# Optimization experiments

Hardware: AMD Instinct MI355X
Metric: run time of the kernel (lower is better)

The kernel has to match this reference:

```python
import jax, jax.numpy as jnp
import numpy as np
import math

B, T, D, N = 4, 1024, 768, 7  # batch, seq, d_model, n_chambers
STEP, WARMUP = 4000, 2000      # curriculum: step past warmup -> all masks ~1
INIT_SCALE = 0.01


def _curriculum_masks():
    # NautilusScheduler.get_masks: smooth sigmoid activation per chamber (static floats)
    slope = 8.0 * N / WARMUP
    return [1.0 / (1.0 + math.exp(-slope * (STEP - WARMUP * (i + 0.5) / N))) for i in range(N)]


def _layernorm(x, g, b, eps=1e-5):
    m = jnp.mean(x, axis=-1, keepdims=True)
    v = jnp.mean((x - m) ** 2, axis=-1, keepdims=True)
    return (x - m) * jax.lax.rsqrt(v + eps) * g + b


def _chamber(h, Wq, Wk, gw, gb, sp, mask_val, causal):
    # get_bias stand-in: bilinear content bias (B,T,T)
    q = h @ Wq                                   # (B,T,D)
    k = h @ Wk                                   # (B,T,D)
    bias = jnp.einsum('btd,bsd->bts', q, k) / jnp.sqrt(jnp.asarray(D, h.dtype))
    bias = jnp.where(causal[None], bias, -jnp.inf)   # causal masked_fill
    w = jnp.nan_to_num(jax.nn.softmax(bias, axis=-1))
    enrichment = jnp.einsum('bts,bsd->btd', w, h) - h
    gate = jax.nn.sigmoid(h @ gw[:, None] + gb)      # (B,T,1)
    scale = jax.nn.softplus(sp)                      # learnable positive scale
    return scale * gate * mask_val * enrichment


def setup_inputs() -> dict:
    key = jax.random.key(0)
    ks = jax.random.split(key, 8)
    x = jax.random.normal(ks[0], (B, T, D), jnp.float32)
    s = 1.0 / np.sqrt(D)
    Wq = jax.random.normal(ks[1], (N, D, D), jnp.float32) * s
    Wk = jax.random.normal(ks[2], (N, D, D), jnp.float32) * s
    gate_w = jax.random.normal(ks[3], (N, D), jnp.float32) * 0.02
    gate_b = jnp.zeros((N,), jnp.float32)
    # per-chamber softplus-inverse init: log(exp(init*(1+3*prog))-1+1e-6)
    sp = np.array([math.log(math.exp(INIT_SCALE * (1.0 + 3.0 * i / (N - 1))) - 1.0 + 1e-6)
                   for i in range(N)], dtype=np.float32)
    scale_p = jnp.asarray(sp)
    merge_W = jax.random.normal(ks[4], (D, N * D), jnp.float32) * (1.0 / np.sqrt(N * D))
    return {
        'x': x, 'Wq': Wq, 'Wk': Wk, 'gate_w': gate_w, 'gate_b': gate_b,
        'scale_p': scale_p, 'merge_W': merge_W,
        'mode_logit': jnp.float32(0.0), 'residual_gate': jnp.float32(0.1),
        'ln_pre_g': jnp.ones((D,), jnp.float32), 'ln_pre_b': jnp.zeros((D,), jnp.float32),
        'ln_post_g': jnp.ones((D,), jnp.float32), 'ln_post_b': jnp.zeros((D,), jnp.float32),
    }


def reference(x, Wq, Wk, gate_w, gate_b, scale_p, merge_W, mode_logit,
              residual_gate, ln_pre_g, ln_pre_b, ln_post_g, ln_post_b):
    masks = _curriculum_masks()
    causal = jnp.tril(jnp.ones((T, T), bool))
    h = _layernorm(x, ln_pre_g, ln_pre_b)
    mode_gate = jax.nn.sigmoid(mode_logit)
    seq = jnp.zeros_like(h)
    deltas = []
    for i in range(N):  # fixed small structural loop over chambers
        seq = seq + _chamber(h + seq, Wq[i], Wk[i], gate_w[i], gate_b[i],
                             scale_p[i], masks[i], causal)
        deltas.append(_chamber(h, Wq[i], Wk[i], gate_w[i], gate_b[i],
                               scale_p[i], masks[i], causal))
    par = jnp.concatenate(deltas, axis=-1) @ merge_W.T  # (B,T,D)
    enrichment = (1.0 - mode_gate) * seq + mode_gate * par
    enrichment = _layernorm(enrichment, ln_post_g, ln_post_b)
    return x + residual_gate * enrichment
```

## Files before the change

kernel.cpp:

```cpp
#include <hip/hip_runtime.h>
#include <hip/hip_bf16.h>
#include <math.h>

#define D_MODEL 768
#define T_SEQ   1024
#define BATCH   4
#define NCH     7
#define ROWS    4096
#define KM      (NCH * D_MODEL)

typedef unsigned short u16;
typedef __attribute__((ext_vector_type(8))) short bh8;
typedef __attribute__((ext_vector_type(4))) float f32x4;

__device__ __forceinline__ u16 f2bf(float f) {
    union { float f; unsigned u; } v; v.f = f;
    return (u16)((v.u + 0x7fffu + ((v.u >> 16) & 1u)) >> 16);
}
__device__ __forceinline__ float bf2f(u16 b) {
    union { unsigned u; float f; } v; v.u = ((unsigned)b) << 16;
    return v.f;
}
__device__ __forceinline__ float wred_sum(float v) {
    #pragma unroll
    for (int o = 32; o; o >>= 1) v += __shfl_down(v, o, 64);
    return v;
}
__device__ __forceinline__ float wred_max(float v) {
    #pragma unroll
    for (int o = 32; o; o >>= 1) v = fmaxf(v, __shfl_down(v, o, 64));
    return v;
}
__device__ __forceinline__ float chamber_mask(int i) {
    float slope = 8.0f * 7.0f / 2000.0f;
    return 1.0f / (1.0f + __expf(-slope * (4000.0f - 2000.0f * (i + 0.5f) / 7.0f)));
}

#define GLD16(g, l) __builtin_amdgcn_global_load_lds( \
    (const __attribute__((address_space(1))) void*)(g), \
    (__attribute__((address_space(3))) void*)(l), 16, 0, 0)

__device__ __forceinline__ int xcd_swizzle(int gflat, int Ntot) {
    if ((Ntot & 7) == 0) {
        int chunk = Ntot >> 3;
        gflat = (gflat & 7) * chunk + (gflat >> 3);
    }
    return gflat;
}

__global__ __launch_bounds__(256)
void gemm_nt_kernel(const u16* __restrict__ A, const u16* __restrict__ B,
                    void* __restrict__ Cv,
                    int K, int lda, int ldb, int ldc,
                    long long sA1, long long sA2, long long sB1, long long sB2,
                    long long sC1, long long sC2, int zm,
                    float alpha, int mode, int causal_skip, int causal_k,
                    int kss, int klen)
{
    int gx = gridDim.x, gy = gridDim.y;
    int Ntot = gx * gy * gridDim.z;
    int gflat = xcd_swizzle(blockIdx.x + gx * (blockIdx.y + gy * blockIdx.z), Ntot);
    int bn = gflat % gx;
    int rest = gflat / gx;
    int bm = rest % gy;
    int bz = rest / gy;
    if (causal_skip && bn > bm) return;
    int bz1 = bz % zm, bz2 = bz / zm;

    const u16* Ab = A + bz1 * sA1 + bz2 * sA2 + (long long)(bm * 128) * lda;
    const u16* Bb = B + bz1 * sB1 + bz2 * sB2 + (long long)(bn * 128) * ldb;

    __shared__ u16 sm[4 * 128 * 32];
    u16* Al0 = sm;
    u16* Bl0 = sm + 128 * 32;
    u16* Al1 = sm + 2 * 128 * 32;
    u16* Bl1 = sm + 3 * 128 * 32;

    int tid  = threadIdx.x;
    int lane = tid & 63;
    int wave = tid >> 6;
    int wm = wave >> 1, wn = wave & 1;

    int k_begin = kss ? bz1 * kss : 0;
    int k_end   = klen ? (k_begin + klen) : K;
    if (causal_k) k_end = min(k_end, (bm + 1) * 128);

    f32x4 acc[4][4];
    #pragma unroll
    for (int i = 0; i < 4; i++)
        #pragma unroll
        for (int j = 0; j < 4; j++)
            acc[i][j] = (f32x4){0.f, 0.f, 0.f, 0.f};

    int srow = lane >> 2;
    int skq  = (lane & 3) * 8;
    int fm   = lane & 15;
    int fk   = (lane >> 4) * 8;

    for (int k0 = k_begin; k0 < k_end; k0 += 64) {
        __syncthreads();
        #pragma unroll
        for (int r = 0; r < 2; r++) {
            int row = r * 64 + wave * 16 + srow;
            long long ra = (long long)row * lda + k0 + skq;
            long long rb2 = (long long)row * ldb + k0 + skq;
            GLD16(Ab + ra,       Al0 + row * 32 + skq);
            GLD16(Bb + rb2,      Bl0 + row * 32 + skq);
            GLD16(Ab + ra + 32,  Al1 + row * 32 + skq);
            GLD16(Bb + rb2 + 32, Bl1 + row * 32 + skq);
        }
        __syncthreads();

        #pragma unroll
        for (int p = 0; p < 2; p++) {
            const u16* Al = p ? Al1 : Al0;
            const u16* Bl = p ? Bl1 : Bl0;
            bh8 af[4], bf[4];
            #pragma unroll
            for (int i = 0; i < 4; i++)
                af[i] = *(const bh8*)(Al + (wm * 64 + i * 16 + fm) * 32 + fk);
            #pragma unroll
            for (int j = 0; j < 4; j++)
                bf[j] = *(const bh8*)(Bl + (wn * 64 + j * 16 + fm) * 32 + fk);
            #pragma unroll
            for (int i = 0; i < 4; i++)
                #pragma unroll
                for (int j = 0; j < 4; j++)
                    acc[i][j] = __builtin_amdgcn_mfma_f32_16x16x32_bf16(af[i], bf[j], acc[i][j], 0, 0, 0);
        }
    }

    int rbase = bm * 128 + wm * 64 + (lane >> 4) * 4;
    int cbase = bn * 128 + wn * 64 + (lane & 15);
    long long zoff = bz1 * sC1 + bz2 * sC2;
    if (mode == 1) {
        u16* C = (u16*)Cv + zoff;
        #pragma unroll
        for (int i = 0; i < 4; i++)
            #pragma unroll
            for (int j = 0; j < 4; j++)
                #pragma unroll
                for (int r = 0; r < 4; r++)
                    C[(long long)(rbase + i * 16 + r) * ldc + cbase + j * 16] = f2bf(acc[i][j][r] * alpha);
    } else if (mode == 3) {
        u16* C = (u16*)Cv + zoff;
        #pragma unroll
        for (int i = 0; i < 4; i++)
            #pragma unroll
            for (int j = 0; j < 4; j++)
                #pragma unroll
                for (int r = 0; r < 4; r++) {
                    union { _Float16 h; u16 u; } cv;
                    cv.h = (_Float16)(acc[i][j][r] * alpha);
                    C[(long long)(rbase + i * 16 + r) * ldc + cbase + j * 16] = cv.u;
                }
    } else {
        float* C = (float*)Cv + zoff;
        #pragma unroll
        for (int i = 0; i < 4; i++)
            #pragma unroll
            for (int j = 0; j < 4; j++)
                #pragma unroll
                for (int r = 0; r < 4; r++)
                    C[(long long)(rbase + i * 16 + r) * ldc + cbase + j * 16] = acc[i][j][r] * alpha;
    }
}

__global__ __launch_bounds__(256)
void gemm64_nt_kernel(const u16* __restrict__ A, const u16* __restrict__ B,
                      void* __restrict__ Cv,
                      int K, int lda, int ldb, int ldc,
                      long long sA1, long long sA2, long long sB1, long long sB2,
                      long long sC1, long long sC2, int zm,
                      float alpha, int mode, int causal_skip, int causal_k,
                      float* __restrict__ hhfp, const float* __restrict__ coefp,
                      u16* __restrict__ hbsp, u16* __restrict__ htsp,
                      const float* __restrict__ hp, u16* __restrict__ dbp)
{
    int gx = gridDim.x, gy = gridDim.y;
    int Ntot = gx * gy * gridDim.z;
    int gflat = xcd_swizzle(blockIdx.x + gx * (blockIdx.y + gy * blockIdx.z), Ntot);
    int bn = gflat % gx;
    int rest = gflat / gx;
    int bm = rest % gy;
    int bz = rest / gy;
    if (causal_skip && bn > bm) return;
    int bz1 = bz % zm, bz2 = bz / zm;

    const u16* Ab = A + bz1 * sA1 + bz2 * sA2 + (long long)(bm * 64) * lda;
    const u16* Bb = B + bz1 * sB1 + bz2 * sB2 + (long long)(bn * 64) * ldb;

    __shared__ u16 sm[8 * 64 * 32];
    const int PS = 64 * 32;

    int tid  = threadIdx.x;
    int lane = tid & 63;
    int wave = tid >> 6;

    int k_end = causal_k ? min(K, (bm + 1) * 64) : K;

    f32x4 acc[4];
    #pragma unroll
    for (int j = 0; j < 4; j++) acc[j] = (f32x4){0.f, 0.f, 0.f, 0.f};

    int srow   = tid >> 2;
    int schunk = (tid & 3) * 8;
    int fm     = lane & 15;
    int fk     = (lane >> 4) * 8;

    int k0 = 0;
    while (k0 < k_end) {
        __syncthreads();
        if (k_end - k0 >= 128) {
            #pragma unroll
            for (int p = 0; p < 4; p++) {
                long long ra  = (long long)srow * lda + k0 + p * 32 + schunk;
                long long rb2 = (long long)srow * ldb + k0 + p * 32 + schunk;
                GLD16(Ab + ra,  sm + (2 * p) * PS + srow * 32 + schunk);
                GLD16(Bb + rb2, sm + (2 * p + 1) * PS + srow * 32 + schunk);
            }
            __syncthreads();
            #pragma unroll
            for (int p = 0; p < 4; p++) {
                const u16* Al = sm + (2 * p) * PS;
                const u16* Bl = sm + (2 * p + 1) * PS;
                bh8 af = *(const bh8*)(Al + (wave * 16 + fm) * 32 + fk);
                bh8 bf[4];
                #pragma unroll
                for (int j = 0; j < 4; j++)
                    bf[j] = *(const bh8*)(Bl + (j * 16 + fm) * 32 + fk);
                #pragma unroll
                for (int j = 0; j < 4; j++)
                    acc[j] = __builtin_amdgcn_mfma_f32_16x16x32_bf16(af, bf[j], acc[j], 0, 0, 0);
            }
            k0 += 128;
        } else {
            #pragma unroll
            for (int p = 0; p < 2; p++) {
                long long ra  = (long long)srow * lda + k0 + p * 32 + schunk;
                long long rb2 = (long long)srow * ldb + k0 + p * 32 + schunk;
                GLD16(Ab + ra,  sm + (2 * p) * PS + srow * 32 + schunk);
                GLD16(Bb + rb2, sm + (2 * p + 1) * PS + srow * 32 + schunk);
            }
            __syncthreads();
            #pragma unroll
            for (int p = 0; p < 2; p++) {
                const u16* Al = sm + (2 * p) * PS;
                const u16* Bl = sm + (2 * p + 1) * PS;
                bh8 af = *(const bh8*)(Al + (wave * 16 + fm) * 32 + fk);
                bh8 bf[4];
                #pragma unroll
                for (int j = 0; j < 4; j++)
                    bf[j] = *(const bh8*)(Bl + (j * 16 + fm) * 32 + fk);
                #pragma unroll
                for (int j = 0; j < 4; j++)
                    acc[j] = __builtin_amdgcn_mfma_f32_16x16x32_bf16(af, bf[j], acc[j], 0, 0, 0);
            }
            k0 += 64;
        }
    }

    int rbase = bm * 64 + wave * 16 + (lane >> 4) * 4;
    int cbase = bn * 64 + (lane & 15);
    long long zoff = bz1 * sC1 + bz2 * sC2;
    if (mode == 1) {
        u16* C = (u16*)Cv + zoff;
        #pragma unroll
        for (int j = 0; j < 4; j++)
            #pragma unroll
            for (int r = 0; r < 4; r++)
                C[(long long)(rbase + r) * ldc + cbase + j * 16] = f2bf(acc[j][r] * alpha);
    } else if (mode == 3) {
        u16* C = (u16*)Cv + zoff;
        #pragma unroll
        for (int j = 0; j < 4; j++)
            #pragma unroll
            for (int r = 0; r < 4; r++) {
                union { _Float16 h; u16 u; } cv;
                cv.h = (_Float16)(acc[j][r] * alpha);
                C[(long long)(rbase + r) * ldc + cbase + j * 16] = cv.u;
            }
    } else if (mode == 5) {
        int b = bz1, ch = bz2;
        #pragma unroll
        for (int r = 0; r < 4; r++) {
            int t = rbase + r;
            long long rowg = (long long)b * T_SEQ + t;
            float cf = coefp[(long long)ch * ROWS + rowg];
            #pragma unroll
            for (int j = 0; j < 4; j++) {
                int d = cbase + j * 16;
                float hv = hp[rowg * D_MODEL + d];
                dbp[rowg * KM + ch * D_MODEL + d] = f2bf(cf * (acc[j][r] - hv));
            }
        }
    } else if (mode == 6) {
        __syncthreads();
        u16* tile = sm;
        #pragma unroll
        for (int r = 0; r < 4; r++) {
            int t = rbase + r;
            long long rowg = (long long)bz1 * T_SEQ + t;
            float cf = coefp[rowg];
            int tl = t - bm * 64;
            #pragma unroll
            for (int j = 0; j < 4; j++) {
                int d = cbase + j * 16;
                long long idx = rowg * D_MODEL + d;
                float v = hhfp[idx];
                float nh = v + cf * (acc[j][r] - v);
                hhfp[idx] = nh;
                u16 w = f2bf(nh);
                hbsp[idx] = w;
                tile[((lane & 15) + j * 16) * 66 + tl] = w;
            }
        }
        __syncthreads();
        int dl = tid >> 2, tch = (tid & 3) * 16;
        long long ob = (long long)bz1 * T_SEQ * D_MODEL +
                       (long long)(bn * 64 + dl) * T_SEQ + bm * 64 + tch;
        #pragma unroll
        for (int kk = 0; kk < 16; kk++)
            htsp[ob + kk] = tile[dl * 66 + tch + kk];
    } else {
        float* C = (float*)Cv + zoff;
        #pragma unroll
        for (int j = 0; j < 4; j++)
            #pragma unroll
            for (int r = 0; r < 4; r++)
                C[(long long)(rbase + r) * ldc + cbase + j * 16] = acc[j][r] * alpha;
    }
}

__global__ __launch_bounds__(256)
void ln_pre_kernel(const float* __restrict__ x, const float* __restrict__ g,
                   const float* __restrict__ b, float* __restrict__ h,
                   float* __restrict__ hhf, u16* __restrict__ hbp,
                   u16* __restrict__ hbs)
{
    int row = blockIdx.x;
    long long base = (long long)row * D_MODEL;
    int tid = threadIdx.x, lane = tid & 63, wave = tid >> 6;
    __shared__ float red[4];
    float v[3]; float s = 0.f;
    #pragma unroll
    for (int k = 0; k < 3; k++) { v[k] = x[base + tid + k * 256]; s += v[k]; }
    s = wred_sum(s);
    if (lane == 0) red[wave] = s;
    __syncthreads();
    float mean = (red[0] + red[1] + red[2] + red[3]) * (1.f / D_MODEL);
    __syncthreads();
    float sq = 0.f;
    #pragma unroll
    for (int k = 0; k < 3; k++) { float dd = v[k] - mean; sq += dd * dd; }
    sq = wred_sum(sq);
    if (lane == 0) red[wave] = sq;
    __syncthreads();
    float var = (red[0] + red[1] + red[2] + red[3]) * (1.f / D_MODEL);
    float rstd = rsqrtf(var + 1e-5f);
    #pragma unroll
    for (int k = 0; k < 3; k++) {
        int c = tid + k * 256;
        float o = (v[k] - mean) * rstd * g[c] + b[c];
        h[base + c] = o; hhf[base + c] = o;
        u16 w = f2bf(o);
        hbp[base + c] = w; hbs[base + c] = w;
    }
}

__global__ __launch_bounds__(256)
void transpose2_kernel(const u16* __restrict__ hb, u16* __restrict__ htp,
                       u16* __restrict__ hts)
{
    __shared__ u16 tile[32][33];
    int b = blockIdx.z;
    int d0 = blockIdx.x * 32, t0 = blockIdx.y * 32;
    int tx = threadIdx.x & 31, ty = threadIdx.x >> 5;
    long long bb = (long long)b * T_SEQ * D_MODEL;
    #pragma unroll
    for (int i = 0; i < 32; i += 8)
        tile[ty + i][tx] = hb[bb + (long long)(t0 + ty + i) * D_MODEL + d0 + tx];
    __syncthreads();
    #pragma unroll
    for (int i = 0; i < 32; i += 8) {
        long long o = bb + (long long)(d0 + ty + i) * T_SEQ + t0 + tx;
        u16 w = tile[tx][ty + i];
        htp[o] = w; hts[o] = w;
    }
}

__device__ __forceinline__ void softmax_row(u16* row, int len, int tid, int lane, int wave,
                                            float* red)
{
    float ev[4];
    float m = -3.0e38f;
    #pragma unroll
    for (int k = 0; k < 4; k++) {
        int s = tid + k * 256;
        if (s < len) {
            union { u16 u; _Float16 h; } cv; cv.u = row[s];
            ev[k] = (float)cv.h;
        } else ev[k] = -3.0e38f;
        m = fmaxf(m, ev[k]);
    }
    m = wred_max(m);
    if (lane == 0) red[wave] = m;
    __syncthreads();
    m = fmaxf(fmaxf(red[0], red[1]), fmaxf(red[2], red[3]));
    __syncthreads();
    float sum = 0.f;
    #pragma unroll
    for (int k = 0; k < 4; k++) {
        int s = tid + k * 256;
        float e = (s < len) ? __expf(ev[k] - m) : 0.f;
        ev[k] = e; sum += e;
    }
    sum = wred_sum(sum);
    if (lane == 0) red[wave] = sum;
    __syncthreads();
    sum = red[0] + red[1] + red[2] + red[3];
    float inv = 1.f / sum;
    #pragma unroll
    for (int k = 0; k < 4; k++)
        row[tid + k * 256] = f2bf(ev[k] * inv);
}

__global__ __launch_bounds__(256)
void softmax_kernel(u16* __restrict__ SP)
{
    int t = blockIdx.x, z = blockIdx.y;
    __shared__ float red[4];
    int tid = threadIdx.x, lane = tid & 63, wave = tid >> 6;
    softmax_row(SP + (long long)z * T_SEQ * T_SEQ + (long long)t * T_SEQ,
                t + 1, tid, lane, wave, red);
}

__global__ __launch_bounds__(256)
void softmax_coef_kernel(u16* __restrict__ SP, const float* __restrict__ hhf,
                         const float* __restrict__ gw, const float* __restrict__ gb,
                         const float* __restrict__ sp, int ci,
                         float* __restrict__ coefS)
{
    int t = blockIdx.x, z = blockIdx.y;
    int tid = threadIdx.x, lane = tid & 63, wave = tid >> 6;
    if (z == BATCH) {
        int row = t * 4 + wave;
        long long base = (long long)row * D_MODEL;
        const float* g = gw + ci * D_MODEL;
        float dot = 0.f;
        #pragma unroll
        for (int k = 0; k < 12; k++) dot += hhf[base + lane + 64 * k] * g[lane + 64 * k];
        dot = wred_sum(dot);
        if (lane == 0) {
            float gate = 1.f / (1.f + __expf(-(dot + gb[ci])));
            coefS[row] = log1pf(expf(sp[ci])) * chamber_mask(ci) * gate;
        }
        return;
    }
    __shared__ float red[4];
    softmax_row(SP + (long long)z * T_SEQ * T_SEQ + (long long)t * T_SEQ,
                t + 1, tid, lane, wave, red);
}

__global__ __launch_bounds__(256)
void coef_par_kernel(const float* __restrict__ h, const float* __restrict__ gw,
                     const float* __restrict__ gb, const float* __restrict__ sp,
                     float* __restrict__ coefP)
{
    int row = blockIdx.x * 4 + (threadIdx.x >> 6);
    int lane = threadIdx.x & 63;
    long long base = (long long)row * D_MODEL;
    float hv[12];
    #pragma unroll
    for (int k = 0; k < 12; k++) hv[k] = h[base + lane + 64 * k];
    for (int ci = 0; ci < NCH; ci++) {
        const float* g = gw + ci * D_MODEL;
        float dot = 0.f;
        #pragma unroll
        for (int k = 0; k < 12; k++) dot += hv[k] * g[lane + 64 * k];
        dot = wred_sum(dot);
        if (lane == 0) {
            float gate = 1.f / (1.f + __expf(-(dot + gb[ci])));
            coefP[ci * ROWS + row] = log1pf(expf(sp[ci])) * chamber_mask(ci) * gate;
        }
    }
}

__global__ __launch_bounds__(256)
void cast4_kernel(const float4* __restrict__ in, ushort4* __restrict__ outp, int n4)
{
    int i = blockIdx.x * 256 + threadIdx.x;
    if (i < n4) {
        float4 v = in[i];
        ushort4 o;
        o.x = f2bf(v.x); o.y = f2bf(v.y); o.z = f2bf(v.z); o.w = f2bf(v.w);
        outp[i] = o;
    }
}

__global__ __launch_bounds__(256)
void final_kernel(const float* __restrict__ x, const float* __restrict__ h,
                  const float* __restrict__ hhf, const u16* __restrict__ Pp,
                  const float* __restrict__ mode_logit, const float* __restrict__ residual_gate,
                  const float* __restrict__ g, const float* __restrict__ b,
                  float* __restrict__ out)
{
    const long long RDe = (long long)ROWS * D_MODEL;
    int row = blockIdx.x;
    long long base = (long long)row * D_MODEL;
    int tid = threadIdx.x, lane = tid & 63, wave = tid >> 6;
    __shared__ float red[4];
    float mg = 1.f / (1.f + __expf(-mode_logit[0]));
    float rg = residual_gate[0];
    float e[3]; float s = 0.f;
    #pragma unroll
    for (int k = 0; k < 3; k++) {
        int c = tid + k * 256;
        float p = 0.f;
        #pragma unroll
        for (int z = 0; z < NCH; z++) p += bf2f(Pp[z * RDe + base + c]);
        float v = (1.f - mg) * (hhf[base + c] - h[base + c]) + mg * p;
        e[k] = v; s += v;
    }
    s = wred_sum(s);
    if (lane == 0) red[wave] = s;
    __syncthreads();
    float mean = (red[0] + red[1] + red[2] + red[3]) * (1.f / D_MODEL);
    __syncthreads();
    float sq = 0.f;
    #pragma unroll
    for (int k = 0; k < 3; k++) { float dd = e[k] - mean; sq += dd * dd; }
    sq = wred_sum(sq);
    if (lane == 0) red[wave] = sq;
    __syncthreads();
    float var = (red[0] + red[1] + red[2] + red[3]) * (1.f / D_MODEL);
    float rstd = rsqrtf(var + 1e-5f);
    #pragma unroll
    for (int k = 0; k < 3; k++) {
        int c = tid + k * 256;
        out[base + c] = x[base + c] + rg * ((e[k] - mean) * rstd * g[c] + b[c]);
    }
}

extern "C" void kernel_launch(void* const* d_in, const int* in_sizes, int n_in,
                              void* d_out, int out_size, void* d_ws, size_t ws_size,
                              hipStream_t stream)
{
    (void)in_sizes; (void)n_in; (void)out_size; (void)ws_size;
    const float* x             = (const float*)d_in[0];
    const float* Wq            = (const float*)d_in[1];
    const float* Wk            = (const float*)d_in[2];
    const float* gate_w        = (const float*)d_in[3];
    const float* gate_b        = (const float*)d_in[4];
    const float* scale_p       = (const float*)d_in[5];
    const float* merge_W       = (const float*)d_in[6];
    const float* mode_logit    = (const float*)d_in[7];
    const float* residual_gate = (const float*)d_in[8];
    const float* ln_pre_g      = (const float*)d_in[9];
    const float* ln_pre_b      = (const float*)d_in[10];
    const float* ln_post_g     = (const float*)d_in[11];
    const float* ln_post_b     = (const float*)d_in[12];
    float* out = (float*)d_out;

    const long long DD  = (long long)D_MODEL * D_MODEL;
    const long long TD  = (long long)T_SEQ * D_MODEL;
    const long long TTs = (long long)T_SEQ * T_SEQ;
    const long long RDe = (long long)ROWS * D_MODEL;

    size_t off = 0;
    char* wsb = (char*)d_ws;
    auto alloc = [&](size_t bytes) -> void* {
        void* p = wsb + off; off += (bytes + 255) & ~(size_t)255; return p;
    };
    u16*   Mtb  = (u16*)alloc((size_t)NCH * DD * 2);
    u16*   mgb  = (u16*)alloc((size_t)D_MODEL * KM * 2);
    float* h    = (float*)alloc(RDe * 4);
    float* hhf  = (float*)alloc(RDe * 4);
    u16*   hbp  = (u16*)alloc(RDe * 2);
    u16*   htp  = (u16*)alloc(RDe * 2);
    u16*   hbs  = (u16*)alloc(RDe * 2);
    u16*   hts0 = (u16*)alloc(RDe * 2);
    u16*   hts1 = (u16*)alloc(RDe * 2);
    u16*   Spar = (u16*)alloc((size_t)(NCH * BATCH) * TTs * 2);
    u16*   Sseq = (u16*)alloc((size_t)BATCH * TTs * 2);
    u16*   Upar = (u16*)alloc((size_t)NCH * RDe * 2);
    u16*   Useq = (u16*)alloc(RDe * 2);
    u16*   db   = (u16*)alloc((size_t)ROWS * KM * 2);
    float* coefP= (float*)alloc((size_t)NCH * ROWS * 4);
    float* coefS= (float*)alloc((size_t)ROWS * 4);
    u16*   Wqb  = Spar;
    u16*   Wkb  = Spar + (size_t)NCH * DD;
    u16*   Pp   = Upar;

    const float sc = 1.0f / sqrtf((float)D_MODEL);
    const int N4W = (int)((size_t)NCH * DD) / 4;
    const int N4M = (int)((size_t)D_MODEL * KM) / 4;

    ln_pre_kernel<<<ROWS, 256, 0, stream>>>(x, ln_pre_g, ln_pre_b, h, hhf, hbp, hbs);
    cast4_kernel<<<(N4W + 255) / 256, 256, 0, stream>>>((const float4*)Wq, (ushort4*)Wqb, N4W);
    cast4_kernel<<<(N4W + 255) / 256, 256, 0, stream>>>((const float4*)Wk, (ushort4*)Wkb, N4W);
    cast4_kernel<<<(N4M + 255) / 256, 256, 0, stream>>>((const float4*)merge_W, (ushort4*)mgb, N4M);
    transpose2_kernel<<<dim3(24, 32, BATCH), 256, 0, stream>>>(hbp, htp, hts0);
    coef_par_kernel<<<ROWS / 4, 256, 0, stream>>>(h, gate_w, gate_b, scale_p, coefP);

    gemm_nt_kernel<<<dim3(6, 6, NCH), 256, 0, stream>>>(
        Wkb, Wqb, Mtb, D_MODEL, D_MODEL, D_MODEL, D_MODEL,
        DD, 0, DD, 0, DD, 0, NCH, 1.f, 1, 0, 0, 0, 0);

    gemm_nt_kernel<<<dim3(6, 32, NCH), 256, 0, stream>>>(
        hbp, Mtb, Upar, D_MODEL, D_MODEL, D_MODEL, D_MODEL,
        0, 0, DD, 0, RDe, 0, NCH, 1.f, 1, 0, 0, 0, 0);
    gemm64_nt_kernel<<<dim3(16, 16, BATCH * NCH), 256, 0, stream>>>(
        Upar, hbp, Spar, D_MODEL, D_MODEL, D_MODEL, T_SEQ,
        TD, RDe, TD, 0, TTs, 4 * TTs, BATCH, sc, 3, 1, 0,
        nullptr, nullptr, nullptr, nullptr, nullptr, nullptr);
    softmax_kernel<<<dim3(T_SEQ, BATCH * NCH), 256, 0, stream>>>(Spar);
    gemm64_nt_kernel<<<dim3(12, 16, BATCH * NCH), 256, 0, stream>>>(
        Spar, htp, nullptr, T_SEQ, T_SEQ, T_SEQ, D_MODEL,
        TTs, 4 * TTs, TD, 0, 0, 0, BATCH, 1.f, 5, 0, 1,
        nullptr, coefP, nullptr, nullptr, h, db);
    gemm_nt_kernel<<<dim3(6, 32, NCH), 256, 0, stream>>>(
        db, mgb, Pp, KM, KM, KM, D_MODEL,
        0, 0, 0, 0, RDe, 0, NCH, 1.f, 1, 0, 0, D_MODEL, D_MODEL);

    u16* htsCur = hts0;
    u16* htsNxt = hts1;
    for (int i = 0; i < NCH; i++) {
        gemm64_nt_kernel<<<dim3(12, 64, 1), 256, 0, stream>>>(
            hbs, Mtb + (long long)i * DD, Useq,
            D_MODEL, D_MODEL, D_MODEL, D_MODEL, 0, 0, 0, 0, 0, 0, 1,
            1.f, 1, 0, 0, nullptr, nullptr, nullptr, nullptr, nullptr, nullptr);
        gemm64_nt_kernel<<<dim3(16, 16, BATCH), 256, 0, stream>>>(
            Useq, hbs, Sseq, D_MODEL, D_MODEL, D_MODEL, T_SEQ,
            TD, 0, TD, 0, TTs, 0, BATCH, sc, 3, 1, 0,
            nullptr, nullptr, nullptr, nullptr, nullptr, nullptr);
        softmax_coef_kernel<<<dim3(T_SEQ, BATCH + 1), 256, 0, stream>>>(
            Sseq, hhf, gate_w, gate_b, scale_p, i, coefS);
        gemm64_nt_kernel<<<dim3(12, 16, BATCH), 256, 0, stream>>>(
            Sseq, htsCur, nullptr, T_SEQ, T_SEQ, T_SEQ, D_MODEL,
            TTs, 0, TD, 0, 0, 0, BATCH, 1.f, 6, 0, 1,
            hhf, coefS, hbs, htsNxt, nullptr, nullptr);
        u16* tmp = htsCur; htsCur = htsNxt; htsNxt = tmp;
    }

    final_kernel<<<ROWS, 256, 0, stream>>>(x, h, hhf, Pp, mode_logit, residual_gate,
                                           ln_post_g, ln_post_b, out);
}
```

Measured before the change: 790.7 us.

## Use 32-row GEMM tiles for sequential chamber loop to raise block count

Adds a gemm32_nt_kernel with 32x64 output tiles and a 2x2 wave layout, and uses it for the three GEMMs inside the sequential per-chamber loop, doubling the grid size so these small serial launches fill more compute units. Causal skipping and the causal K bound are adapted to the finer row granularity. The 64-tile kernel's K loop is collapsed into a single runtime-count loop, and its mode 6 path moves to the new kernel. Smaller tiles halve MFMA work per block and lower data reuse, and the non-unrolled p loop may cost some instruction scheduling.

```diff
diff --git a/kernel.cpp b/kernel.cpp
--- a/kernel.cpp
+++ b/kernel.cpp
@@ -173,8 +173,7 @@
                       long long sA1, long long sA2, long long sB1, long long sB2,
                       long long sC1, long long sC2, int zm,
                       float alpha, int mode, int causal_skip, int causal_k,
-                      float* __restrict__ hhfp, const float* __restrict__ coefp,
-                      u16* __restrict__ hbsp, u16* __restrict__ htsp,
+                      const float* __restrict__ coefp,
                       const float* __restrict__ hp, u16* __restrict__ dbp)
 {
     int gx = gridDim.x, gy = gridDim.y;
@@ -211,53 +210,27 @@
     int k0 = 0;
     while (k0 < k_end) {
         __syncthreads();
-        if (k_end - k0 >= 128) {
-            #pragma unroll
-            for (int p = 0; p < 4; p++) {
-                long long ra  = (long long)srow * lda + k0 + p * 32 + schunk;
-                long long rb2 = (long long)srow * ldb + k0 + p * 32 + schunk;
-                GLD16(Ab + ra,  sm + (2 * p) * PS + srow * 32 + schunk);
-                GLD16(Bb + rb2, sm + (2 * p + 1) * PS + srow * 32 + schunk);
-            }
-            __syncthreads();
-            #pragma unroll
-            for (int p = 0; p < 4; p++) {
-                const u16* Al = sm + (2 * p) * PS;
-                const u16* Bl = sm + (2 * p + 1) * PS;
-                bh8 af = *(const bh8*)(Al + (wave * 16 + fm) * 32 + fk);
-                bh8 bf[4];
-                #pragma unroll
-                for (int j = 0; j < 4; j++)
-                    bf[j] = *(const bh8*)(Bl + (j * 16 + fm) * 32 + fk);
-                #pragma unroll
-                for (int j = 0; j < 4; j++)
-                    acc[j] = __builtin_amdgcn_mfma_f32_16x16x32_bf16(af, bf[j], acc[j], 0, 0, 0);
-            }
-            k0 += 128;
-        } else {
-            #pragma unroll
-            for (int p = 0; p < 2; p++) {
-                long long ra  = (long long)srow * lda + k0 + p * 32 + schunk;
-                long long rb2 = (long long)srow * ldb + k0 + p * 32 + schunk;
-                GLD16(Ab + ra,  sm + (2 * p) * PS + srow * 32 + schunk);
-                GLD16(Bb + rb2, sm + (2 * p + 1) * PS + srow * 32 + schunk);
-            }
-            __syncthreads();
-            #pragma unroll
-            for (int p = 0; p < 2; p++) {
-                const u16* Al = sm + (2 * p) * PS;
-                const u16* Bl = sm + (2 * p + 1) * PS;
-                bh8 af = *(const bh8*)(Al + (wave * 16 + fm) * 32 + fk);
-                bh8 bf[4];
-                #pragma unroll
-                for (int j = 0; j < 4; j++)
-                    bf[j] = *(const bh8*)(Bl + (j * 16 + fm) * 32 + fk);
-                #pragma unroll
-                for (int j = 0; j < 4; j++)
-                    acc[j] = __builtin_amdgcn_mfma_f32_16x16x32_bf16(af, bf[j], acc[j], 0, 0, 0);
-            }
-            k0 += 64;
-        }
+        int np = (k_end - k0 >= 128) ? 4 : 2;
+        for (int p = 0; p < np; p++) {
+            long long ra  = (long long)srow * lda + k0 + p * 32 + schunk;
+            long long rb2 = (long long)srow * ldb + k0 + p * 32 + schunk;
+            GLD16(Ab + ra,  sm + (2 * p) * PS + srow * 32 + schunk);
+            GLD16(Bb + rb2, sm + (2 * p + 1) * PS + srow * 32 + schunk);
+        }
+        __syncthreads();
+        for (int p = 0; p < np; p++) {
+            const u16* Al = sm + (2 * p) * PS;
+            const u16* Bl = sm + (2 * p + 1) * PS;
+            bh8 af = *(const bh8*)(Al + (wave * 16 + fm) * 32 + fk);
+            bh8 bf[4];
+            #pragma unroll
+            for (int j = 0; j < 4; j++)
+                bf[j] = *(const bh8*)(Bl + (j * 16 + fm) * 32 + fk);
+            #pragma unroll
+            for (int j = 0; j < 4; j++)
+                acc[j] = __builtin_amdgcn_mfma_f32_16x16x32_bf16(af, bf[j], acc[j], 0, 0, 0);
+        }
+        k0 += np * 32;
     }
 
     int rbase = bm * 64 + wave * 16 + (lane >> 4) * 4;
@@ -294,6 +267,109 @@
                 dbp[rowg * KM + ch * D_MODEL + d] = f2bf(cf * (acc[j][r] - hv));
             }
         }
+    } else {
+        float* C = (float*)Cv + zoff;
+        #pragma unroll
+        for (int j = 0; j < 4; j++)
+            #pragma unroll
+            for (int r = 0; r < 4; r++)
+                C[(long long)(rbase + r) * ldc + cbase + j * 16] = acc[j][r] * alpha;
+    }
+}
+
+__global__ __launch_bounds__(256)
+void gemm32_nt_kernel(const u16* __restrict__ A, const u16* __restrict__ B,
+                      void* __restrict__ Cv,
+                      int K, int lda, int ldb, int ldc,
+                      long long sA1, long long sB1, long long sC1, int zm,
+                      float alpha, int mode, int causal_skip, int causal_k,
+                      float* __restrict__ hhfp, const float* __restrict__ coefp,
+                      u16* __restrict__ hbsp, u16* __restrict__ htsp)
+{
+    int gx = gridDim.x, gy = gridDim.y;
+    int Ntot = gx * gy * gridDim.z;
+    int gflat = xcd_swizzle(blockIdx.x + gx * (blockIdx.y + gy * blockIdx.z), Ntot);
+    int bn = gflat % gx;
+    int rest = gflat / gx;
+    int bm = rest % gy;
+    int bz1 = rest / gy;
+    (void)zm;
+    if (causal_skip && bn * 64 > bm * 32 + 31) return;
+
+    const u16* Ab = A + bz1 * sA1 + (long long)(bm * 32) * lda;
+    const u16* Bb = B + bz1 * sB1 + (long long)(bn * 64) * ldb;
+
+    __shared__ u16 sm[4 * 96 * 32];
+    const int PS = 96 * 32;
+
+    int tid  = threadIdx.x;
+    int lane = tid & 63;
+    int wave = tid >> 6;
+    int wm = wave & 1, wn = wave >> 1;
+
+    int k_end = K;
+    if (causal_k) {
+        int ke = bm * 32 + 32;
+        ke = (ke + 63) & ~63;
+        k_end = min(K, ke);
+    }
+
+    f32x4 acc[2];
+    acc[0] = (f32x4){0.f, 0.f, 0.f, 0.f};
+    acc[1] = (f32x4){0.f, 0.f, 0.f, 0.f};
+
+    int srow   = tid >> 2;
+    int schunk = (tid & 3) * 8;
+    int fm     = lane & 15;
+    int fk     = (lane >> 4) * 8;
+
+    int k0 = 0;
+    while (k0 < k_end) {
+        __syncthreads();
+        int np = (k_end - k0 >= 128) ? 4 : 2;
+        for (int p = 0; p < np; p++) {
+            if (tid < 128)
+                GLD16(Ab + (long long)srow * lda + k0 + p * 32 + schunk,
+                      sm + p * PS + srow * 32 + schunk);
+            GLD16(Bb + (long long)srow * ldb + k0 + p * 32 + schunk,
+                  sm + p * PS + 32 * 32 + srow * 32 + schunk);
+        }
+        __syncthreads();
+        for (int p = 0; p < np; p++) {
+            const u16* Al = sm + p * PS;
+            const u16* Bl = sm + p * PS + 32 * 32;
+            bh8 af = *(const bh8*)(Al + (wm * 16 + fm) * 32 + fk);
+            bh8 bf[2];
+            #pragma unroll
+            for (int j = 0; j < 2; j++)
+                bf[j] = *(const bh8*)(Bl + (wn * 32 + j * 16 + fm) * 32 + fk);
+            #pragma unroll
+            for (int j = 0; j < 2; j++)
+                acc[j] = __builtin_amdgcn_mfma_f32_16x16x32_bf16(af, bf[j], acc[j], 0, 0, 0);
+        }
+        k0 += np * 32;
+    }
+
+    int rbase = bm * 32 + wm * 16 + (lane >> 4) * 4;
+    int cbase = bn * 64 + wn * 32 + (lane & 15);
+    long long zoff = bz1 * sC1;
+    if (mode == 1) {
+        u16* C = (u16*)Cv + zoff;
+        #pragma unroll
+        for (int j = 0; j < 2; j++)
+            #pragma unroll
+            for (int r = 0; r < 4; r++)
+                C[(long long)(rbase + r) * ldc + cbase + j * 16] = f2bf(acc[j][r] * alpha);
+    } else if (mode == 3) {
+        u16* C = (u16*)Cv + zoff;
+        #pragma unroll
+        for (int j = 0; j < 2; j++)
+            #pragma unroll
+            for (int r = 0; r < 4; r++) {
+                union { _Float16 h; u16 u; } cv;
+                cv.h = (_Float16)(acc[j][r] * alpha);
+                C[(long long)(rbase + r) * ldc + cbase + j * 16] = cv.u;
+            }
     } else if (mode == 6) {
         __syncthreads();
         u16* tile = sm;
@@ -302,9 +378,9 @@
             int t = rbase + r;
             long long rowg = (long long)bz1 * T_SEQ + t;
             float cf = coefp[rowg];
-            int tl = t - bm * 64;
-            #pragma unroll
-            for (int j = 0; j < 4; j++) {
+            int tl = t - bm * 32;
+            #pragma unroll
+            for (int j = 0; j < 2; j++) {
                 int d = cbase + j * 16;
                 long long idx = rowg * D_MODEL + d;
                 float v = hhfp[idx];
@@ -312,23 +388,17 @@
                 hhfp[idx] = nh;
                 u16 w = f2bf(nh);
                 hbsp[idx] = w;
-                tile[((lane & 15) + j * 16) * 66 + tl] = w;
+                int dl = d - bn * 64;
+                tile[dl * 34 + tl] = w;
             }
         }
         __syncthreads();
-        int dl = tid >> 2, tch = (tid & 3) * 16;
+        int dl = tid >> 2, tt = (tid & 3) * 8;
         long long ob = (long long)bz1 * T_SEQ * D_MODEL +
-                       (long long)(bn * 64 + dl) * T_SEQ + bm * 64 + tch;
-        #pragma unroll
-        for (int kk = 0; kk < 16; kk++)
-            htsp[ob + kk] = tile[dl * 66 + tch + kk];
-    } else {
-        float* C = (float*)Cv + zoff;
-        #pragma unroll
-        for (int j = 0; j < 4; j++)
-            #pragma unroll
-            for (int r = 0; r < 4; r++)
-                C[(long long)(rbase + r) * ldc + cbase + j * 16] = acc[j][r] * alpha;
+                       (long long)(bn * 64 + dl) * T_SEQ + bm * 32 + tt;
+        #pragma unroll
+        for (int kk = 0; kk < 8; kk++)
+            htsp[ob + kk] = tile[dl * 34 + tt + kk];
     }
 }
 
@@ -613,12 +683,12 @@
     gemm64_nt_kernel<<<dim3(16, 16, BATCH * NCH), 256, 0, stream>>>(
         Upar, hbp, Spar, D_MODEL, D_MODEL, D_MODEL, T_SEQ,
         TD, RDe, TD, 0, TTs, 4 * TTs, BATCH, sc, 3, 1, 0,
-        nullptr, nullptr, nullptr, nullptr, nullptr, nullptr);
+        nullptr, nullptr, nullptr);
     softmax_kernel<<<dim3(T_SEQ, BATCH * NCH), 256, 0, stream>>>(Spar);
     gemm64_nt_kernel<<<dim3(12, 16, BATCH * NCH), 256, 0, stream>>>(
         Spar, htp, nullptr, T_SEQ, T_SEQ, T_SEQ, D_MODEL,
         TTs, 4 * TTs, TD, 0, 0, 0, BATCH, 1.f, 5, 0, 1,
-        nullptr, coefP, nullptr, nullptr, h, db);
+        coefP, h, db);
     gemm_nt_kernel<<<dim3(6, 32, NCH), 256, 0, stream>>>(
         db, mgb, Pp, KM, KM, KM, D_MODEL,
         0, 0, 0, 0, RDe, 0, NCH, 1.f, 1, 0, 0, D_MODEL, D_MODEL);
@@ -626,20 +696,20 @@
     u16* htsCur = hts0;
     u16* htsNxt = hts1;
     for (int i = 0; i < NCH; i++) {
-        gemm64_nt_kernel<<<dim3(12, 64, 1), 256, 0, stream>>>(
+        gemm32_nt_kernel<<<dim3(12, 128, 1), 256, 0, stream>>>(
             hbs, Mtb + (long long)i * DD, Useq,
-            D_MODEL, D_MODEL, D_MODEL, D_MODEL, 0, 0, 0, 0, 0, 0, 1,
-            1.f, 1, 0, 0, nullptr, nullptr, nullptr, nullptr, nullptr, nullptr);
-        gemm64_nt_kernel<<<dim3(16, 16, BATCH), 256, 0, stream>>>(
+            D_MODEL, D_MODEL, D_MODEL, D_MODEL, 0, 0, 0, 1,
+            1.f, 1, 0, 0, nullptr, nullptr, nullptr, nullptr);
+        gemm32_nt_kernel<<<dim3(16, 32, BATCH), 256, 0, stream>>>(
             Useq, hbs, Sseq, D_MODEL, D_MODEL, D_MODEL, T_SEQ,
-            TD, 0, TD, 0, TTs, 0, BATCH, sc, 3, 1, 0,
-            nullptr, nullptr, nullptr, nullptr, nullptr, nullptr);
+            TD, TD, TTs, BATCH, sc, 3, 1, 0,
+            nullptr, nullptr, nullptr, nullptr);
         softmax_coef_kernel<<<dim3(T_SEQ, BATCH + 1), 256, 0, stream>>>(
             Sseq, hhf, gate_w, gate_b, scale_p, i, coefS);
-        gemm64_nt_kernel<<<dim3(12, 16, BATCH), 256, 0, stream>>>(
+        gemm32_nt_kernel<<<dim3(12, 32, BATCH), 256, 0, stream>>>(
             Sseq, htsCur, nullptr, T_SEQ, T_SEQ, T_SEQ, D_MODEL,
-            TTs, 0, TD, 0, 0, 0, BATCH, 1.f, 6, 0, 1,
-            hhf, coefS, hbs, htsNxt, nullptr, nullptr);
+            TTs, TD, 0, BATCH, 1.f, 6, 0, 1,
+            hhf, coefS, hbs, htsNxt);
         u16* tmp = htsCur; htsCur = htsNxt; htsNxt = tmp;
     }
 
```

After: 854.3 us. 1.08x slower.
